# Kernel tuning notes

Measured on AMD Instinct MI355X. Metric: run time of the kernel, lower is better.

The kernel has to match this reference:

```python
import jax, jax.numpy as jnp
import numpy as np

# Static config (matches init_kwargs / docstring example)
SHAPES = ((100, 100), (50, 50), (25, 25), (13, 13))  # (H, W) per level
L, P, NH, HD, E, F = 4, 4, 8, 32, 256, 1024
NUM_LAYERS = 6
EPS = 1e-5
NUM_KEYS = sum(h * w for h, w in SHAPES)  # 13294


def _ln(x, g, b):
    m = jnp.mean(x, -1, keepdims=True)
    v = jnp.var(x, -1, keepdims=True)
    return (x - m) * jax.lax.rsqrt(v + EPS) * g + b


def _ms_deform_attn(value, loc, aw):
    # value: (B,N,NH,HD)  loc: (B,N,NH,L,P,2) normalized  aw: (B,N,NH,L,P)
    B, N = value.shape[:2]
    out = jnp.zeros((B, NH, N, HD), value.dtype)
    start = 0
    for lvl, (h, w) in enumerate(SHAPES):
        v = value[:, start:start + h * w].transpose(0, 2, 1, 3)  # (B,NH,hw,HD)
        start += h * w
        # grid_sample align_corners=False pixel coords
        x = loc[:, :, :, lvl, :, 0] * w - 0.5  # (B,N,NH,P)
        y = loc[:, :, :, lvl, :, 1] * h - 0.5
        x0 = jnp.floor(x); y0 = jnp.floor(y)
        lx = x - x0; ly = y - y0
        x0 = x0.astype(jnp.int32); y0 = y0.astype(jnp.int32)

        def gather(yi, xi):
            valid = ((xi >= 0) & (xi < w) & (yi >= 0) & (yi < h)).astype(value.dtype)
            idx = jnp.clip(yi, 0, h - 1) * w + jnp.clip(xi, 0, w - 1)  # (B,N,NH,P)
            idx = idx.transpose(0, 2, 1, 3).reshape(B, NH, N * P, 1)
            got = jnp.take_along_axis(v, idx, axis=2).reshape(B, NH, N, P, HD)
            return got * valid.transpose(0, 2, 1, 3)[..., None]

        def wgt(a):  # (B,N,NH,P) -> (B,NH,N,P,1)
            return a.transpose(0, 2, 1, 3)[..., None]

        samp = (gather(y0, x0) * wgt((1 - lx) * (1 - ly))
                + gather(y0, x0 + 1) * wgt(lx * (1 - ly))
                + gather(y0 + 1, x0) * wgt((1 - lx) * ly)
                + gather(y0 + 1, x0 + 1) * wgt(lx * ly))  # (B,NH,N,P,HD)
        out = out + jnp.sum(samp * wgt(aw[:, :, :, lvl]), axis=3)
    return out.transpose(0, 2, 1, 3).reshape(B, N, NH * HD)


def _layer(x, ref, Woff, boff, Waw, baw, Wv, bv, Wo, bo, ln1_g, ln1_b, Wf1, bf1, Wf2, bf2, ln2_g, ln2_b):
    B, N, _ = x.shape
    v = (x @ Wv + bv).reshape(B, N, NH, HD)
    off = (x @ Woff + boff).reshape(B, N, NH, L, P, 2)
    aw = jax.nn.softmax((x @ Waw + baw).reshape(B, N, NH, L * P), -1).reshape(B, N, NH, L, P)
    normalizer = jnp.asarray([[w, h] for (h, w) in SHAPES], x.dtype)  # (L,2) in (x,y)=(W,H)
    loc = ref[:, :, None, :, None, :] + off / normalizer[None, None, None, :, None, :]
    attn = _ms_deform_attn(v, loc, aw) @ Wo + bo
    x = _ln(x + attn, ln1_g, ln1_b)
    f = jax.nn.relu(x @ Wf1 + bf1) @ Wf2 + bf2
    return _ln(x + f, ln2_g, ln2_b)


def setup_inputs() -> dict:
    key = jax.random.key(0)
    ks = jax.random.split(key, 10)
    s = 0.02
    return {
        "src": jax.random.normal(ks[0], (2, NUM_KEYS, E), jnp.float32),
        "reference_points": jax.random.uniform(ks[1], (2, NUM_KEYS, L, 2), jnp.float32),
        "spatial_shapes": jnp.asarray(SHAPES, jnp.int32),
        "level_start_index": jnp.asarray([0, 10000, 12500, 13125], jnp.int32),
        "Woff": jax.random.normal(ks[2], (E, NH * L * P * 2), jnp.float32) * s,
        "boff": jnp.zeros((NH * L * P * 2,), jnp.float32),
        "Waw": jax.random.normal(ks[3], (E, NH * L * P), jnp.float32) * s,
        "baw": jnp.zeros((NH * L * P,), jnp.float32),
        "Wv": jax.random.normal(ks[4], (E, E), jnp.float32) * s,
        "bv": jnp.zeros((E,), jnp.float32),
        "Wo": jax.random.normal(ks[5], (E, E), jnp.float32) * s,
        "bo": jnp.zeros((E,), jnp.float32),
        "ln1_g": jnp.ones((E,), jnp.float32),
        "ln1_b": jnp.zeros((E,), jnp.float32),
        "Wf1": jax.random.normal(ks[6], (E, F), jnp.float32) * s,
        "bf1": jnp.zeros((F,), jnp.float32),
        "Wf2": jax.random.normal(ks[7], (F, E), jnp.float32) * s,
        "bf2": jnp.zeros((E,), jnp.float32),
        "ln2_g": jnp.ones((E,), jnp.float32),
        "ln2_b": jnp.zeros((E,), jnp.float32),
    }


def reference(src, reference_points, spatial_shapes, level_start_index, Woff, boff, Waw, baw, Wv, bv, Wo, bo, ln1_g, ln1_b, Wf1, bf1, Wf2, bf2, ln2_g, ln2_b):
    # NOTE: the torch encoder reuses the SAME layer object num_layers times,
    # so parameters are shared across all 6 layers.
    x = src
    for _ in range(NUM_LAYERS):
        x = _layer(x, reference_points, Woff, boff, Waw, baw, Wv, bv, Wo, bo,
                   ln1_g, ln1_b, Wf1, bf1, Wf2, bf2, ln2_g, ln2_b)
    return x
```

## Files before the change

kernel.cpp:

```cpp
#include <hip/hip_runtime.h>
#include <hip/hip_bf16.h>
#include <math.h>

#define NKEYS 13294
#define BATCH 2
#define MROWS (BATCH * NKEYS)
#define EDIM  256
#define FDIM  1024
#define EPSV  1e-5f

typedef __bf16 bf16x8 __attribute__((ext_vector_type(8)));
typedef float  f32x4  __attribute__((ext_vector_type(4)));
typedef float  f32x2  __attribute__((ext_vector_type(2)));

__device__ __forceinline__ void async16(const void* g, void* l) {
    __builtin_amdgcn_global_load_lds(
        (const __attribute__((address_space(1))) void*)g,
        (__attribute__((address_space(3))) void*)l, 16, 0, 0);
}

template<int MODE>
__global__ __launch_bounds__(256, 4) void gemm_mfma_k(
    const __hip_bfloat16* __restrict__ A, const __hip_bfloat16* __restrict__ WT,
    const float* __restrict__ bias, __hip_bfloat16* __restrict__ Cout,
    int M, int N, int K,
    __hip_bfloat16* __restrict__ o_vb, __hip_bfloat16* __restrict__ o_off,
    __hip_bfloat16* __restrict__ o_aw)
{
    constexpr int BM = 128, BN = 128, BKc = 32;
    constexpr int SMX = (BM + BN) * BKc;
    __shared__ __hip_bfloat16 smem[2 * SMX];

    const int gx = gridDim.x, nb = gx * gridDim.y;
    int bxi = blockIdx.x, byi = blockIdx.y;
    if ((nb & 7) == 0) {
        const int id   = byi * gx + bxi;
        const int tile = (id & 7) * (nb >> 3) + (id >> 3);
        bxi = tile % gx; byi = tile / gx;
    }
    const int bm = byi * BM;
    const int bn = bxi * BN;

    const int tid  = threadIdx.x;
    const int lane = tid & 63;
    const int w    = tid >> 6;
    const int wr   = w >> 1, wc = w & 1;
    const int l15  = lane & 15, quad = lane >> 4;

    const int gRow = tid >> 2;
    const int kc8  = (tid & 3) * 8;
    const __hip_bfloat16* gsrc[4];
    int ldsoff[4];
    #pragma unroll
    for (int rr = 0; rr < 4; ++rr) {
        const int gr = gRow + 64 * rr;
        if (gr < BM) {
            int ar = bm + gr; if (ar >= M) ar = M - 1;
            gsrc[rr] = A + (size_t)ar * K + kc8;
        } else {
            gsrc[rr] = WT + (size_t)(bn + gr - BM) * K + kc8;
        }
        ldsoff[rr] = gr * BKc + kc8;
    }

    f32x4 acc[4][4];
    #pragma unroll
    for (int i = 0; i < 4; ++i)
        #pragma unroll
        for (int j = 0; j < 4; ++j) acc[i][j] = (f32x4)0.f;

    const int T = K / BKc;
    #pragma unroll
    for (int rr = 0; rr < 4; ++rr) async16(gsrc[rr], smem + ldsoff[rr]);

    for (int it = 0; it < T; ++it) {
        __syncthreads();
        if (it + 1 < T) {
            const int nxt = ((it + 1) & 1) * SMX;
            const int ko  = (it + 1) * BKc;
            #pragma unroll
            for (int rr = 0; rr < 4; ++rr) async16(gsrc[rr] + ko, smem + nxt + ldsoff[rr]);
        }
        const __hip_bfloat16* sA = smem + (it & 1) * SMX;
        const __hip_bfloat16* sB = sA + BM * BKc;

        bf16x8 a[4], b[4];
        #pragma unroll
        for (int mt = 0; mt < 4; ++mt)
            a[mt] = *(const bf16x8*)&sA[(wr * 64 + mt * 16 + l15) * BKc + quad * 8];
        #pragma unroll
        for (int nt = 0; nt < 4; ++nt)
            b[nt] = *(const bf16x8*)&sB[(wc * 64 + nt * 16 + l15) * BKc + quad * 8];
        #pragma unroll
        for (int mt = 0; mt < 4; ++mt)
            #pragma unroll
            for (int nt = 0; nt < 4; ++nt)
                acc[mt][nt] = __builtin_amdgcn_mfma_f32_16x16x32_bf16(
                    b[nt], a[mt], acc[mt][nt], 0, 0, 0);
    }

    #pragma unroll
    for (int nt = 0; nt < 4; ++nt) {
        const int col = bn + wc * 64 + nt * 16 + quad * 4;
        const float4 bz = *(const float4*)&bias[col];
        #pragma unroll
        for (int mt = 0; mt < 4; ++mt) {
            const int row = bm + wr * 64 + mt * 16 + l15;
            if (row >= M) continue;
            float v0 = acc[mt][nt][0] + bz.x;
            float v1 = acc[mt][nt][1] + bz.y;
            float v2 = acc[mt][nt][2] + bz.z;
            float v3 = acc[mt][nt][3] + bz.w;
            if (MODE == 3) {
                v0 = fmaxf(v0, 0.f); v1 = fmaxf(v1, 0.f);
                v2 = fmaxf(v2, 0.f); v3 = fmaxf(v3, 0.f);
            }
            union { uint2 u; __hip_bfloat16 h[4]; } p;
            p.h[0] = __float2bfloat16(v0); p.h[1] = __float2bfloat16(v1);
            p.h[2] = __float2bfloat16(v2); p.h[3] = __float2bfloat16(v3);
            if (MODE == 1) {
                if (col < 256) {
                    const int bb = (row >= NKEYS) ? 1 : 0;
                    const int hh = col >> 5, d = col & 31;
                    *(uint2*)&o_vb[((size_t)(bb * 7 + hh) * NKEYS + row) * 32 + d] = p.u;
                } else if (col < 512) {
                    *(uint2*)&o_off[(size_t)row * 256 + (col - 256)] = p.u;
                } else {
                    *(uint2*)&o_aw[(size_t)row * 128 + (col - 512)] = p.u;
                }
            } else {
                *(uint2*)&Cout[(size_t)row * N + col] = p.u;
            }
        }
    }
}

template<int FINAL>
__global__ __launch_bounds__(256, 2) void gemm_ln_k(
    const __hip_bfloat16* __restrict__ A, const __hip_bfloat16* __restrict__ WT,
    const float* __restrict__ bias, const __hip_bfloat16* __restrict__ xres,
    const float* __restrict__ g, const float* __restrict__ bta,
    float* __restrict__ xfout, __hip_bfloat16* __restrict__ xbout,
    int M, int K)
{
    constexpr int BM = 64, BN = 256, BKc = 32;
    constexpr int ROWS = BM + BN;
    constexpr int SMX = ROWS * BKc;
    __shared__ __hip_bfloat16 smem[2 * SMX];

    const int tid  = threadIdx.x;
    const int bm   = blockIdx.x * BM;
    const int lane = tid & 63;
    const int w    = tid >> 6;
    const int l15  = lane & 15, quad = lane >> 4;

    const int gRow = tid >> 2;
    const int kc8  = (tid & 3) * 8;
    const __hip_bfloat16* gsrc[5];
    int ldsoff[5];
    #pragma unroll
    for (int rr = 0; rr < 5; ++rr) {
        const int gr = gRow + 64 * rr;
        if (gr < BM) {
            int ar = bm + gr; if (ar >= M) ar = M - 1;
            gsrc[rr] = A + (size_t)ar * K + kc8;
        } else {
            gsrc[rr] = WT + (size_t)(gr - BM) * K + kc8;
        }
        ldsoff[rr] = gr * BKc + kc8;
    }

    f32x4 acc[4][4];
    #pragma unroll
    for (int i = 0; i < 4; ++i)
        #pragma unroll
        for (int j = 0; j < 4; ++j) acc[i][j] = (f32x4)0.f;

    const int T = K / BKc;
    #pragma unroll
    for (int rr = 0; rr < 5; ++rr) async16(gsrc[rr], smem + ldsoff[rr]);

    for (int it = 0; it < T; ++it) {
        __syncthreads();
        if (it + 1 < T) {
            const int nxt = ((it + 1) & 1) * SMX;
            const int ko  = (it + 1) * BKc;
            #pragma unroll
            for (int rr = 0; rr < 5; ++rr) async16(gsrc[rr] + ko, smem + nxt + ldsoff[rr]);
        }
        const __hip_bfloat16* sA = smem + (it & 1) * SMX;
        const __hip_bfloat16* sB = sA + BM * BKc;

        bf16x8 a[4], b[4];
        #pragma unroll
        for (int mt = 0; mt < 4; ++mt)
            a[mt] = *(const bf16x8*)&sA[(mt * 16 + l15) * BKc + quad * 8];
        #pragma unroll
        for (int nt = 0; nt < 4; ++nt)
            b[nt] = *(const bf16x8*)&sB[(w * 64 + nt * 16 + l15) * BKc + quad * 8];
        #pragma unroll
        for (int mt = 0; mt < 4; ++mt)
            #pragma unroll
            for (int nt = 0; nt < 4; ++nt)
                acc[mt][nt] = __builtin_amdgcn_mfma_f32_16x16x32_bf16(
                    b[nt], a[mt], acc[mt][nt], 0, 0, 0);
    }

    const int colq = w * 64 + quad * 4;

    #pragma unroll
    for (int nt = 0; nt < 4; ++nt) {
        const int col = colq + nt * 16;
        const float4 bz = *(const float4*)&bias[col];
        #pragma unroll
        for (int mt = 0; mt < 4; ++mt) {
            int row = bm + mt * 16 + l15;
            if (row >= M) row = M - 1;
            const ushort4 xr = *(const ushort4*)&xres[(size_t)row * 256 + col];
            acc[mt][nt][0] += bz.x + __uint_as_float((unsigned)xr.x << 16);
            acc[mt][nt][1] += bz.y + __uint_as_float((unsigned)xr.y << 16);
            acc[mt][nt][2] += bz.z + __uint_as_float((unsigned)xr.z << 16);
            acc[mt][nt][3] += bz.w + __uint_as_float((unsigned)xr.w << 16);
        }
    }

    __syncthreads();
    float* stats = (float*)smem;
    #pragma unroll
    for (int mt = 0; mt < 4; ++mt) {
        float s = 0.f, sq = 0.f;
        #pragma unroll
        for (int nt = 0; nt < 4; ++nt)
            #pragma unroll
            for (int r = 0; r < 4; ++r) {
                const float v = acc[mt][nt][r];
                s += v; sq += v * v;
            }
        s  += __shfl_xor(s,  16, 64);  s  += __shfl_xor(s,  32, 64);
        sq += __shfl_xor(sq, 16, 64);  sq += __shfl_xor(sq, 32, 64);
        if (quad == 0) {
            const int rl = mt * 16 + l15;
            stats[(w * 64 + rl) * 2 + 0] = s;
            stats[(w * 64 + rl) * 2 + 1] = sq;
        }
    }
    __syncthreads();

    #pragma unroll
    for (int mt = 0; mt < 4; ++mt) {
        const int rl  = mt * 16 + l15;
        const int row = bm + rl;
        float s  = stats[rl * 2]          + stats[(64 + rl) * 2]
                 + stats[(128 + rl) * 2]  + stats[(192 + rl) * 2];
        float sq = stats[rl * 2 + 1]      + stats[(64 + rl) * 2 + 1]
                 + stats[(128 + rl) * 2 + 1] + stats[(192 + rl) * 2 + 1];
        const float mean = s * (1.f / 256.f);
        const float var  = sq * (1.f / 256.f) - mean * mean;
        const float rstd = rsqrtf(var + EPSV);
        if (row < M) {
            #pragma unroll
            for (int nt = 0; nt < 4; ++nt) {
                const int col = colq + nt * 16;
                const float4 gz  = *(const float4*)&g[col];
                const float4 bb4 = *(const float4*)&bta[col];
                const float v0 = (acc[mt][nt][0] - mean) * rstd * gz.x + bb4.x;
                const float v1 = (acc[mt][nt][1] - mean) * rstd * gz.y + bb4.y;
                const float v2 = (acc[mt][nt][2] - mean) * rstd * gz.z + bb4.z;
                const float v3 = (acc[mt][nt][3] - mean) * rstd * gz.w + bb4.w;
                union { uint2 u; __hip_bfloat16 h[4]; } p;
                p.h[0] = __float2bfloat16(v0); p.h[1] = __float2bfloat16(v1);
                p.h[2] = __float2bfloat16(v2); p.h[3] = __float2bfloat16(v3);
                *(uint2*)&xbout[(size_t)row * 256 + col] = p.u;
                if (FINAL) {
                    float4 f; f.x = v0; f.y = v1; f.z = v2; f.w = v3;
                    *(float4*)&xfout[(size_t)row * 256 + col] = f;
                }
            }
        }
    }
}

template<int FINAL>
__global__ __launch_bounds__(256, 2) void ffn_fused_k(
    const __hip_bfloat16* __restrict__ xin,
    const __hip_bfloat16* __restrict__ WTf1,
    const __hip_bfloat16* __restrict__ WTf2,
    const float* __restrict__ bf1, const float* __restrict__ bf2,
    const float* __restrict__ g, const float* __restrict__ bta,
    float* __restrict__ xfout, __hip_bfloat16* __restrict__ xbout,
    int M)
{
    __shared__ __hip_bfloat16 xs[8 * 64 * 32];
    __shared__ __hip_bfloat16 ps[2 * 2 * 64 * 32];

    const int tid  = threadIdx.x;
    const int bm   = blockIdx.x * 64;
    const int lane = tid & 63;
    const int w    = tid >> 6;
    const int l15  = lane & 15, quad = lane >> 4;

    {
        const int gr  = tid >> 2;
        const int kc8 = (tid & 3) * 8;
        int ar = bm + gr; if (ar >= M) ar = M - 1;
        const __hip_bfloat16* src = xin + (size_t)ar * 256 + kc8;
        #pragma unroll
        for (int kt = 0; kt < 8; ++kt)
            async16(src + kt * 32, xs + (kt * 64 + gr) * 32 + kc8);
    }

    f32x4 acc[4][4];
    #pragma unroll
    for (int i = 0; i < 4; ++i)
        #pragma unroll
        for (int j = 0; j < 4; ++j) acc[i][j] = (f32x4)0.f;

    __syncthreads();

    const int kt2w = w >> 1;
    const int kcw  = (w & 1) * 16 + quad * 4;

    for (int nf = 0; nf < 16; ++nf) {
        const int buf = nf & 1;

        bf16x8 bw[8];
        {
            const __hip_bfloat16* wp =
                WTf1 + (size_t)(nf * 64 + w * 16 + l15) * 256 + quad * 8;
            #pragma unroll
            for (int kt = 0; kt < 8; ++kt) bw[kt] = *(const bf16x8*)(wp + kt * 32);
        }
        f32x4 pacc[4];
        #pragma unroll
        for (int mt = 0; mt < 4; ++mt) pacc[mt] = (f32x4)0.f;
        #pragma unroll
        for (int kt = 0; kt < 8; ++kt) {
            #pragma unroll
            for (int mt = 0; mt < 4; ++mt) {
                const bf16x8 a = *(const bf16x8*)&xs[(kt * 64 + mt * 16 + l15) * 32 + quad * 8];
                pacc[mt] = __builtin_amdgcn_mfma_f32_16x16x32_bf16(bw[kt], a, pacc[mt], 0, 0, 0);
            }
        }
        {
            const float4 bz = *(const float4*)&bf1[nf * 64 + w * 16 + quad * 4];
            #pragma unroll
            for (int mt = 0; mt < 4; ++mt) {
                union { uint2 u; __hip_bfloat16 h[4]; } p;
                p.h[0] = __float2bfloat16(fmaxf(pacc[mt][0] + bz.x, 0.f));
                p.h[1] = __float2bfloat16(fmaxf(pacc[mt][1] + bz.y, 0.f));
                p.h[2] = __float2bfloat16(fmaxf(pacc[mt][2] + bz.z, 0.f));
                p.h[3] = __float2bfloat16(fmaxf(pacc[mt][3] + bz.w, 0.f));
                *(uint2*)&ps[((buf * 2 + kt2w) * 64 + mt * 16 + l15) * 32 + kcw] = p.u;
            }
        }
        __syncthreads();

        const __hip_bfloat16* wp2 =
            WTf2 + (size_t)(w * 64 + l15) * 1024 + nf * 64 + quad * 8;
        #pragma unroll
        for (int kt2 = 0; kt2 < 2; ++kt2) {
            bf16x8 b2[4];
            #pragma unroll
            for (int nt = 0; nt < 4; ++nt)
                b2[nt] = *(const bf16x8*)(wp2 + (size_t)nt * 16 * 1024 + kt2 * 32);
            #pragma unroll
            for (int mt = 0; mt < 4; ++mt) {
                const bf16x8 a = *(const bf16x8*)&ps[((buf * 2 + kt2) * 64 + mt * 16 + l15) * 32 + quad * 8];
                #pragma unroll
                for (int nt = 0; nt < 4; ++nt)
                    acc[mt][nt] = __builtin_amdgcn_mfma_f32_16x16x32_bf16(
                        b2[nt], a, acc[mt][nt], 0, 0, 0);
            }
        }
    }

    const int colq = w * 64 + quad * 4;
    #pragma unroll
    for (int nt = 0; nt < 4; ++nt) {
        const int col = colq + nt * 16;
        const float4 bz = *(const float4*)&bf2[col];
        const int ktr = col >> 5, kcr = col & 31;
        #pragma unroll
        for (int mt = 0; mt < 4; ++mt) {
            const int row = mt * 16 + l15;
            const ushort4 xr = *(const ushort4*)&xs[(ktr * 64 + row) * 32 + kcr];
            acc[mt][nt][0] += bz.x + __uint_as_float((unsigned)xr.x << 16);
            acc[mt][nt][1] += bz.y + __uint_as_float((unsigned)xr.y << 16);
            acc[mt][nt][2] += bz.z + __uint_as_float((unsigned)xr.z << 16);
            acc[mt][nt][3] += bz.w + __uint_as_float((unsigned)xr.w << 16);
        }
    }

    __syncthreads();
    float* stats = (float*)ps;
    #pragma unroll
    for (int mt = 0; mt < 4; ++mt) {
        float s = 0.f, sq = 0.f;
        #pragma unroll
        for (int nt = 0; nt < 4; ++nt)
            #pragma unroll
            for (int r = 0; r < 4; ++r) {
                const float v = acc[mt][nt][r];
                s += v; sq += v * v;
            }
        s  += __shfl_xor(s,  16, 64);  s  += __shfl_xor(s,  32, 64);
        sq += __shfl_xor(sq, 16, 64);  sq += __shfl_xor(sq, 32, 64);
        if (quad == 0) {
            const int rl = mt * 16 + l15;
            stats[(w * 64 + rl) * 2 + 0] = s;
            stats[(w * 64 + rl) * 2 + 1] = sq;
        }
    }
    __syncthreads();

    #pragma unroll
    for (int mt = 0; mt < 4; ++mt) {
        const int rl  = mt * 16 + l15;
        const int row = bm + rl;
        float s  = stats[rl * 2]          + stats[(64 + rl) * 2]
                 + stats[(128 + rl) * 2]  + stats[(192 + rl) * 2];
        float sq = stats[rl * 2 + 1]      + stats[(64 + rl) * 2 + 1]
                 + stats[(128 + rl) * 2 + 1] + stats[(192 + rl) * 2 + 1];
        const float mean = s * (1.f / 256.f);
        const float var  = sq * (1.f / 256.f) - mean * mean;
        const float rstd = rsqrtf(var + EPSV);
        if (row < M) {
            #pragma unroll
            for (int nt = 0; nt < 4; ++nt) {
                const int col = colq + nt * 16;
                const float4 gz  = *(const float4*)&g[col];
                const float4 bb4 = *(const float4*)&bta[col];
                const float v0 = (acc[mt][nt][0] - mean) * rstd * gz.x + bb4.x;
                const float v1 = (acc[mt][nt][1] - mean) * rstd * gz.y + bb4.y;
                const float v2 = (acc[mt][nt][2] - mean) * rstd * gz.z + bb4.z;
                const float v3 = (acc[mt][nt][3] - mean) * rstd * gz.w + bb4.w;
                union { uint2 u; __hip_bfloat16 h[4]; } p;
                p.h[0] = __float2bfloat16(v0); p.h[1] = __float2bfloat16(v1);
                p.h[2] = __float2bfloat16(v2); p.h[3] = __float2bfloat16(v3);
                *(uint2*)&xbout[(size_t)row * 256 + col] = p.u;
                if (FINAL) {
                    float4 f; f.x = v0; f.y = v1; f.z = v2; f.w = v3;
                    *(float4*)&xfout[(size_t)row * 256 + col] = f;
                }
            }
        }
    }
}

__global__ void convert_wt_k(const float* __restrict__ W, __hip_bfloat16* __restrict__ WT,
                             int K, int N, int rowOff)
{
    const int idx = blockIdx.x * 256 + threadIdx.x;
    if (idx >= K * N) return;
    const int k = idx / N, n = idx % N;
    WT[(size_t)(rowOff + n) * K + k] = __float2bfloat16(W[idx]);
}

__global__ void pack_bias_k(const float* __restrict__ bv, const float* __restrict__ boff,
                            const float* __restrict__ baw, float* __restrict__ dst)
{
    const int i = blockIdx.x * 256 + threadIdx.x;
    if (i < 256) dst[i] = bv[i];
    else if (i < 512) dst[i] = boff[i - 256];
    else if (i < 640) dst[i] = baw[i - 512];
}

__global__ void convert_src_k(const float* __restrict__ src, __hip_bfloat16* __restrict__ xb)
{
    const int i = blockIdx.x * 256 + threadIdx.x;
    const float4 v = ((const float4*)src)[i];
    xb[i * 4 + 0] = __float2bfloat16(v.x);
    xb[i * 4 + 1] = __float2bfloat16(v.y);
    xb[i * 4 + 2] = __float2bfloat16(v.z);
    xb[i * 4 + 3] = __float2bfloat16(v.w);
}

__global__ __launch_bounds__(256) void sample_k(
    const __hip_bfloat16* __restrict__ v_bf,
    const __hip_bfloat16* __restrict__ offb,
    const __hip_bfloat16* __restrict__ awb,
    const float* __restrict__ ref,
    __hip_bfloat16* __restrict__ out)
{
    __shared__ alignas(16) float sw[272][4];
    __shared__ alignas(16) int   sa[272][4];
    const int t  = threadIdx.x;
    const int q0 = blockIdx.x * 2;
    const int qi = t >> 7, h = (t >> 4) & 7;

    {
        const int i = t & 15;
        const int q = q0 + qi;
        const int l = i >> 2;
        const float logit = __bfloat162float(awb[(size_t)q * 128 + h * 16 + i]);
        float mx = logit;
        #pragma unroll
        for (int m = 1; m < 16; m <<= 1) mx = fmaxf(mx, __shfl_xor(mx, m, 64));
        const float e = __expf(logit - mx);
        float s = e;
        #pragma unroll
        for (int m = 1; m < 16; m <<= 1) s += __shfl_xor(s, m, 64);
        const float aw = e / s;

        const int ww = (l == 0) ? 100 : (l == 1) ? 50 : (l == 2) ? 25 : 13;
        const int ls = (l == 0) ? 0 : (l == 1) ? 10000 : (l == 2) ? 12500 : 13125;
        const int b  = (q >= NKEYS) ? 1 : 0;
        const int slab = (b * 8 + h) * NKEYS + ls;

        const __hip_bfloat162 ofp = *(const __hip_bfloat162*)&offb[(size_t)q * 256 + h * 32 + i * 2];
        const float2 rf = *(const float2*)&ref[(size_t)q * 8 + l * 2];
        const float x = rf.x * (float)ww + __bfloat162float(ofp.x) - 0.5f;
        const float y = rf.y * (float)ww + __bfloat162float(ofp.y) - 0.5f;
        const float x0f = floorf(x), y0f = floorf(y);
        const float lx = x - x0f, ly = y - y0f;
        const int x0 = (int)x0f, y0 = (int)y0f;
        const bool x0ok = (x0 >= 0) & (x0 < ww);
        const bool x1ok = (x0 + 1 >= 0) & (x0 + 1 < ww);
        const bool y0ok = (y0 >= 0) & (y0 < ww);
        const bool y1ok = (y0 + 1 >= 0) & (y0 + 1 < ww);

        float w00 = (1.f - lx) * (1.f - ly) * aw;
        float w01 = lx * (1.f - ly) * aw;
        float w10 = (1.f - lx) * ly * aw;
        float w11 = lx * ly * aw;
        int a00 = slab + y0 * ww + x0;
        int a01 = a00 + 1;
        int a10 = a00 + ww;
        int a11 = a10 + 1;
        if (!(y0ok & x0ok)) { w00 = 0.f; a00 = 0; }
        if (!(y0ok & x1ok)) { w01 = 0.f; a01 = 0; }
        if (!(y1ok & x0ok)) { w10 = 0.f; a10 = 0; }
        if (!(y1ok & x1ok)) { w11 = 0.f; a11 = 0; }

        const int idx = (qi * 8 + h) * 17 + i;
        sw[idx][0] = w00; sw[idx][1] = w01; sw[idx][2] = w10; sw[idx][3] = w11;
        sa[idx][0] = a00 * 64; sa[idx][1] = a01 * 64;
        sa[idx][2] = a10 * 64; sa[idx][3] = a11 * 64;
    }
    __syncthreads();

    const int d2 = t & 15;
    const unsigned d4 = d2 * 4;
    const char* vb = (const char*)v_bf;
    const int ebase = (qi * 8 + h) * 17;
    f32x2 acc = (f32x2)0.f;
    #pragma unroll
    for (int i = 0; i < 16; ++i) {
        const f32x4 wv = *(const f32x4*)sw[ebase + i];
        const int4  av = *(const int4*)sa[ebase + i];
        const unsigned p0 = *(const unsigned*)(vb + ((unsigned)av.x + d4));
        const unsigned p1 = *(const unsigned*)(vb + ((unsigned)av.y + d4));
        const unsigned p2 = *(const unsigned*)(vb + ((unsigned)av.z + d4));
        const unsigned p3 = *(const unsigned*)(vb + ((unsigned)av.w + d4));
        f32x2 v;
        v[0] = __uint_as_float(p0 << 16); v[1] = __uint_as_float(p0 & 0xffff0000u);
        acc += (f32x2)(wv[0]) * v;
        v[0] = __uint_as_float(p1 << 16); v[1] = __uint_as_float(p1 & 0xffff0000u);
        acc += (f32x2)(wv[1]) * v;
        v[0] = __uint_as_float(p2 << 16); v[1] = __uint_as_float(p2 & 0xffff0000u);
        acc += (f32x2)(wv[2]) * v;
        v[0] = __uint_as_float(p3 << 16); v[1] = __uint_as_float(p3 & 0xffff0000u);
        acc += (f32x2)(wv[3]) * v;
    }
    __hip_bfloat162 ov;
    ov.x = __float2bfloat16(acc[0]);
    ov.y = __float2bfloat16(acc[1]);
    *(__hip_bfloat162*)&out[(size_t)(q0 + qi) * 256 + h * 32 + d2 * 2] = ov;
}

extern "C" void kernel_launch(void* const* d_in, const int* in_sizes, int n_in,
                              void* d_out, int out_size, void* d_ws, size_t ws_size,
                              hipStream_t stream)
{
    const float* src  = (const float*)d_in[0];
    const float* ref  = (const float*)d_in[1];
    const float* Woff = (const float*)d_in[4];
    const float* boff = (const float*)d_in[5];
    const float* Waw  = (const float*)d_in[6];
    const float* baw  = (const float*)d_in[7];
    const float* Wv   = (const float*)d_in[8];
    const float* bv   = (const float*)d_in[9];
    const float* Wo   = (const float*)d_in[10];
    const float* bo   = (const float*)d_in[11];
    const float* ln1g = (const float*)d_in[12];
    const float* ln1b = (const float*)d_in[13];
    const float* Wf1  = (const float*)d_in[14];
    const float* bf1  = (const float*)d_in[15];
    const float* Wf2  = (const float*)d_in[16];
    const float* bf2  = (const float*)d_in[17];
    const float* ln2g = (const float*)d_in[18];
    const float* ln2b = (const float*)d_in[19];

    float* x = (float*)d_out;

    float* ws = (float*)d_ws;
    float* bias1 = ws;
    __hip_bfloat16* v_bf  = (__hip_bfloat16*)(bias1 + 640);
    __hip_bfloat16* offb  = v_bf  + (size_t)MROWS * 256;
    __hip_bfloat16* awb   = offb  + (size_t)MROWS * 256;
    __hip_bfloat16* xb    = awb   + (size_t)MROWS * 128;
    __hip_bfloat16* attnb = xb    + (size_t)MROWS * 256;
    __hip_bfloat16* WT1   = attnb + (size_t)MROWS * 256;
    __hip_bfloat16* WTo   = WT1   + 640 * 256;
    __hip_bfloat16* WTf1  = WTo   + 256 * 256;
    __hip_bfloat16* WTf2  = WTf1  + 1024 * 256;

    convert_wt_k<<<(256 * 256 + 255) / 256, 256, 0, stream>>>(Wv,   WT1,  256, 256,   0);
    convert_wt_k<<<(256 * 256 + 255) / 256, 256, 0, stream>>>(Woff, WT1,  256, 256, 256);
    convert_wt_k<<<(256 * 128 + 255) / 256, 256, 0, stream>>>(Waw,  WT1,  256, 128, 512);
    convert_wt_k<<<(256 * 256 + 255) / 256, 256, 0, stream>>>(Wo,   WTo,  256, 256,   0);
    convert_wt_k<<<(256 * 1024 + 255) / 256, 256, 0, stream>>>(Wf1, WTf1, 256, 1024,  0);
    convert_wt_k<<<(1024 * 256 + 255) / 256, 256, 0, stream>>>(Wf2, WTf2, 1024, 256,  0);
    pack_bias_k<<<3, 256, 0, stream>>>(bv, boff, baw, bias1);
    convert_src_k<<<(MROWS * 64 + 255) / 256, 256, 0, stream>>>(src, xb);

    const int gy  = (MROWS + 127) / 128;
    const int gln = (MROWS + 63) / 64;
    for (int layer = 0; layer < 6; ++layer) {
        gemm_mfma_k<1><<<dim3(640 / 128, gy), 256, 0, stream>>>(
            xb, WT1, bias1, nullptr, MROWS, 640, 256, v_bf, offb, awb);
        sample_k<<<MROWS / 2, 256, 0, stream>>>(v_bf, offb, awb, ref, attnb);
        gemm_ln_k<0><<<gln, 256, 0, stream>>>(
            attnb, WTo, bo, xb, ln1g, ln1b, nullptr, xb, MROWS, 256);
        if (layer < 5)
            ffn_fused_k<0><<<gln, 256, 0, stream>>>(
                xb, WTf1, WTf2, bf1, bf2, ln2g, ln2b, nullptr, xb, MROWS);
        else
            ffn_fused_k<1><<<gln, 256, 0, stream>>>(
                xb, WTf1, WTf2, bf1, bf2, ln2g, ln2b, x, xb, MROWS);
    }
}
```

Baseline: 1.058 ms.

## Halve fused FFN row tile to 32 with XOR-swizzled LDS and hoisted W2 loads

The fused FFN kernel now processes 32 rows per block instead of 64, doubling the grid size. The shared-memory layout for the input rows and the ReLU intermediate is changed to 64-wide rows with an XOR swizzle, to avoid LDS bank conflicts. The second-GEMM weight fragments are loaded before the first GEMM so their latency overlaps with compute. In exchange, each loaded weight tile is reused across half as many rows, which doubles the total weight traffic from L2.

Result: slower. 1.374 ms (+29.9%).

```diff
diff --git a/kernel.cpp b/kernel.cpp
--- a/kernel.cpp
+++ b/kernel.cpp
@@ -290,35 +290,32 @@
     float* __restrict__ xfout, __hip_bfloat16* __restrict__ xbout,
     int M)
 {
-    __shared__ __hip_bfloat16 xs[8 * 64 * 32];
-    __shared__ __hip_bfloat16 ps[2 * 2 * 64 * 32];
+    __shared__ __hip_bfloat16 xs[4 * 32 * 64];
+    __shared__ __hip_bfloat16 ps[2 * 32 * 64];
 
     const int tid  = threadIdx.x;
-    const int bm   = blockIdx.x * 64;
+    const int bm   = blockIdx.x * 32;
     const int lane = tid & 63;
     const int w    = tid >> 6;
     const int l15  = lane & 15, quad = lane >> 4;
 
     {
-        const int gr  = tid >> 2;
-        const int kc8 = (tid & 3) * 8;
-        int ar = bm + gr; if (ar >= M) ar = M - 1;
-        const __hip_bfloat16* src = xin + (size_t)ar * 256 + kc8;
-        #pragma unroll
-        for (int kt = 0; kt < 8; ++kt)
-            async16(src + kt * 32, xs + (kt * 64 + gr) * 32 + kc8);
-    }
-
-    f32x4 acc[4][4];
-    #pragma unroll
-    for (int i = 0; i < 4; ++i)
+        const int slot = tid & 7;
+        const int row  = tid >> 3;
+        int ar = bm + row; if (ar >= M) ar = M - 1;
+        const __hip_bfloat16* src = xin + (size_t)ar * 256 + ((slot ^ (row & 7)) * 8);
+        #pragma unroll
+        for (int kt2 = 0; kt2 < 4; ++kt2)
+            async16(src + kt2 * 64, xs + (kt2 * 32 + row) * 64 + slot * 8);
+    }
+
+    f32x4 acc[2][4];
+    #pragma unroll
+    for (int i = 0; i < 2; ++i)
         #pragma unroll
         for (int j = 0; j < 4; ++j) acc[i][j] = (f32x4)0.f;
 
     __syncthreads();
-
-    const int kt2w = w >> 1;
-    const int kcw  = (w & 1) * 16 + quad * 4;
 
     for (int nf = 0; nf < 16; ++nf) {
         const int buf = nf & 1;
@@ -330,46 +327,59 @@
             #pragma unroll
             for (int kt = 0; kt < 8; ++kt) bw[kt] = *(const bf16x8*)(wp + kt * 32);
         }
-        f32x4 pacc[4];
-        #pragma unroll
-        for (int mt = 0; mt < 4; ++mt) pacc[mt] = (f32x4)0.f;
+        bf16x8 b2[2][4];
+        {
+            const __hip_bfloat16* wp2 =
+                WTf2 + (size_t)(w * 64 + l15) * 1024 + nf * 64 + quad * 8;
+            #pragma unroll
+            for (int kt2 = 0; kt2 < 2; ++kt2)
+                #pragma unroll
+                for (int nt = 0; nt < 4; ++nt)
+                    b2[kt2][nt] = *(const bf16x8*)(wp2 + (size_t)nt * 16 * 1024 + kt2 * 32);
+        }
+
+        f32x4 pacc[2];
+        pacc[0] = (f32x4)0.f; pacc[1] = (f32x4)0.f;
         #pragma unroll
         for (int kt = 0; kt < 8; ++kt) {
-            #pragma unroll
-            for (int mt = 0; mt < 4; ++mt) {
-                const bf16x8 a = *(const bf16x8*)&xs[(kt * 64 + mt * 16 + l15) * 32 + quad * 8];
+            const int kt2 = kt >> 1;
+            const int slotb = (kt & 1) * 4 + quad;
+            #pragma unroll
+            for (int mt = 0; mt < 2; ++mt) {
+                const int m = mt * 16 + l15;
+                const bf16x8 a = *(const bf16x8*)
+                    &xs[(kt2 * 32 + m) * 64 + ((slotb ^ (m & 7)) * 8)];
                 pacc[mt] = __builtin_amdgcn_mfma_f32_16x16x32_bf16(bw[kt], a, pacc[mt], 0, 0, 0);
             }
         }
         {
             const float4 bz = *(const float4*)&bf1[nf * 64 + w * 16 + quad * 4];
-            #pragma unroll
-            for (int mt = 0; mt < 4; ++mt) {
+            const int n0 = w * 16 + quad * 4;
+            #pragma unroll
+            for (int mt = 0; mt < 2; ++mt) {
+                const int row = mt * 16 + l15;
                 union { uint2 u; __hip_bfloat16 h[4]; } p;
                 p.h[0] = __float2bfloat16(fmaxf(pacc[mt][0] + bz.x, 0.f));
                 p.h[1] = __float2bfloat16(fmaxf(pacc[mt][1] + bz.y, 0.f));
                 p.h[2] = __float2bfloat16(fmaxf(pacc[mt][2] + bz.z, 0.f));
                 p.h[3] = __float2bfloat16(fmaxf(pacc[mt][3] + bz.w, 0.f));
-                *(uint2*)&ps[((buf * 2 + kt2w) * 64 + mt * 16 + l15) * 32 + kcw] = p.u;
+                const int sl = ((n0 >> 3) ^ (row & 7));
+                *(uint2*)&ps[(buf * 32 + row) * 64 + sl * 8 + (n0 & 7)] = p.u;
             }
         }
         __syncthreads();
 
-        const __hip_bfloat16* wp2 =
-            WTf2 + (size_t)(w * 64 + l15) * 1024 + nf * 64 + quad * 8;
         #pragma unroll
         for (int kt2 = 0; kt2 < 2; ++kt2) {
-            bf16x8 b2[4];
-            #pragma unroll
-            for (int nt = 0; nt < 4; ++nt)
-                b2[nt] = *(const bf16x8*)(wp2 + (size_t)nt * 16 * 1024 + kt2 * 32);
-            #pragma unroll
-            for (int mt = 0; mt < 4; ++mt) {
-                const bf16x8 a = *(const bf16x8*)&ps[((buf * 2 + kt2) * 64 + mt * 16 + l15) * 32 + quad * 8];
+            #pragma unroll
+            for (int mt = 0; mt < 2; ++mt) {
+                const int m = mt * 16 + l15;
+                const int sl = ((kt2 * 4 + quad) ^ (m & 7));
+                const bf16x8 a = *(const bf16x8*)&ps[(buf * 32 + m) * 64 + sl * 8];
                 #pragma unroll
                 for (int nt = 0; nt < 4; ++nt)
                     acc[mt][nt] = __builtin_amdgcn_mfma_f32_16x16x32_bf16(
-                        b2[nt], a, acc[mt][nt], 0, 0, 0);
+                        b2[kt2][nt], a, acc[mt][nt], 0, 0, 0);
             }
         }
     }
@@ -379,11 +389,13 @@
     for (int nt = 0; nt < 4; ++nt) {
         const int col = colq + nt * 16;
         const float4 bz = *(const float4*)&bf2[col];
-        const int ktr = col >> 5, kcr = col & 31;
-        #pragma unroll
-        for (int mt = 0; mt < 4; ++mt) {
+        const int kt2r = col >> 6, cl = col & 63;
+        #pragma unroll
+        for (int mt = 0; mt < 2; ++mt) {
             const int row = mt * 16 + l15;
-            const ushort4 xr = *(const ushort4*)&xs[(ktr * 64 + row) * 32 + kcr];
+            const int sl = ((cl >> 3) ^ (row & 7));
+            const ushort4 xr = *(const ushort4*)
+                &xs[(kt2r * 32 + row) * 64 + sl * 8 + (cl & 7)];
             acc[mt][nt][0] += bz.x + __uint_as_float((unsigned)xr.x << 16);
             acc[mt][nt][1] += bz.y + __uint_as_float((unsigned)xr.y << 16);
             acc[mt][nt][2] += bz.z + __uint_as_float((unsigned)xr.z << 16);
@@ -394,7 +406,7 @@
     __syncthreads();
     float* stats = (float*)ps;
     #pragma unroll
-    for (int mt = 0; mt < 4; ++mt) {
+    for (int mt = 0; mt < 2; ++mt) {
         float s = 0.f, sq = 0.f;
         #pragma unroll
         for (int nt = 0; nt < 4; ++nt)
@@ -407,20 +419,20 @@
         sq += __shfl_xor(sq, 16, 64);  sq += __shfl_xor(sq, 32, 64);
         if (quad == 0) {
             const int rl = mt * 16 + l15;
-            stats[(w * 64 + rl) * 2 + 0] = s;
-            stats[(w * 64 + rl) * 2 + 1] = sq;
+            stats[(w * 32 + rl) * 2 + 0] = s;
+            stats[(w * 32 + rl) * 2 + 1] = sq;
         }
     }
     __syncthreads();
 
     #pragma unroll
-    for (int mt = 0; mt < 4; ++mt) {
+    for (int mt = 0; mt < 2; ++mt) {
         const int rl  = mt * 16 + l15;
         const int row = bm + rl;
-        float s  = stats[rl * 2]          + stats[(64 + rl) * 2]
-                 + stats[(128 + rl) * 2]  + stats[(192 + rl) * 2];
-        float sq = stats[rl * 2 + 1]      + stats[(64 + rl) * 2 + 1]
-                 + stats[(128 + rl) * 2 + 1] + stats[(192 + rl) * 2 + 1];
+        float s  = stats[rl * 2]         + stats[(32 + rl) * 2]
+                 + stats[(64 + rl) * 2]  + stats[(96 + rl) * 2];
+        float sq = stats[rl * 2 + 1]     + stats[(32 + rl) * 2 + 1]
+                 + stats[(64 + rl) * 2 + 1] + stats[(96 + rl) * 2 + 1];
         const float mean = s * (1.f / 256.f);
         const float var  = sq * (1.f / 256.f) - mean * mean;
         const float rstd = rsqrtf(var + EPSV);
@@ -616,6 +628,7 @@
 
     const int gy  = (MROWS + 127) / 128;
     const int gln = (MROWS + 63) / 64;
+    const int gfn = (MROWS + 31) / 32;
     for (int layer = 0; layer < 6; ++layer) {
         gemm_mfma_k<1><<<dim3(640 / 128, gy), 256, 0, stream>>>(
             xb, WT1, bias1, nullptr, MROWS, 640, 256, v_bf, offb, awb);
@@ -623,10 +636,10 @@
         gemm_ln_k<0><<<gln, 256, 0, stream>>>(
             attnb, WTo, bo, xb, ln1g, ln1b, nullptr, xb, MROWS, 256);
         if (layer < 5)
-            ffn_fused_k<0><<<gln, 256, 0, stream>>>(
+            ffn_fused_k<0><<<gfn, 256, 0, stream>>>(
                 xb, WTf1, WTf2, bf1, bf2, ln2g, ln2b, nullptr, xb, MROWS);
         else
-            ffn_fused_k<1><<<gln, 256, 0, stream>>>(
+            ffn_fused_k<1><<<gfn, 256, 0, stream>>>(
                 xb, WTf1, WTf2, bf1, bf2, ln2g, ln2b, x, xb, MROWS);
     }
 }
```
